# Kernel tuning notes

Hardware: AMD Instinct MI355X
Metric: run time of the kernel (lower is better)

Reference implementation:

```python
import jax, jax.numpy as jnp
import numpy as np

C_, A_, B_ = 1, 128, 128          # image_size
H, Z, T, N = 512, 128, 16, 32     # h_dim, z_dim, steps, attention grid
EPS = 1e-8
BATCH = 256
PATCH = C_ * N * N                # read/write patch size (C_=1)
IN_ENC = 2 * PATCH + H


def gru_cell(x, h, W_ih, W_hh, b_ih, b_hh):
    gi = x @ W_ih.T + b_ih
    gh = h @ W_hh.T + b_hh
    i_r, i_z, i_n = jnp.split(gi, 3, axis=-1)
    h_r, h_z, h_n = jnp.split(gh, 3, axis=-1)
    r = jax.nn.sigmoid(i_r + h_r)
    z = jax.nn.sigmoid(i_z + h_z)
    n = jnp.tanh(i_n + r * h_n)
    return (1.0 - z) * n + z * h


def filterbank(gt, delta, two_sigma_sq, num_pixels):
    # gt, delta: [b,1]; two_sigma_sq: [b,1,1]
    g = 0.5 * (num_pixels + 1) * (gt + 1.0)                       # [b,1]
    grid = jnp.arange(N, dtype=jnp.float32) - 0.5 * (N - 1)       # [N]
    mu = g + grid[None, :] * delta                                # [b,N]
    pix = jnp.arange(num_pixels, dtype=jnp.float32)               # [P]
    F = jnp.exp(-(pix[None, None, :] - mu[:, :, None]) ** 2 / two_sigma_sq)
    return F / jnp.maximum(F.sum(axis=-1, keepdims=True), EPS)    # [b,N,P]


def get_filterbanks(h_dec, W_attn, b_attn):
    p = h_dec @ W_attn.T + b_attn                                 # [b,5]
    gt_x, gt_y, log_ss, log_dt, log_g = [p[:, i:i + 1] for i in range(5)]
    two_sigma_sq = (2.0 * jnp.exp(log_ss))[:, :, None]            # [b,1,1]
    delta = (max(A_, B_) - 1) * jnp.exp(log_dt) / (N - 1)         # [b,1]
    gamma = jnp.exp(log_g)                                        # [b,1]
    F_x = filterbank(gt_x, delta, two_sigma_sq, A_)               # [b,N,A]
    F_y = filterbank(gt_y, delta, two_sigma_sq, B_)               # [b,N,B]
    return F_x, F_y, gamma


def draw_forward(x, eps, W_ih_enc, W_hh_enc, b_ih_enc, b_hh_enc,
                 W_ih_dec, W_hh_dec, b_ih_dec, b_hh_dec,
                 W_mu, b_mu, W_ls, b_ls, W_wr, b_wr,
                 W_ra, b_ra, W_wa, b_wa):
    b = x.shape[0]
    xf = x.reshape(b, -1)                                         # [b, A*B]
    reconsts0 = jnp.zeros_like(xf)
    h0 = jnp.zeros((b, H), dtype=xf.dtype)

    def step(carry, eps_t):
        reconsts, h_enc, h_dec = carry
        # NOTE: faithful to original: reconsts[-1] is last batch row, broadcast
        x_hat = xf - jax.nn.sigmoid(reconsts[-1])
        # ---- read with attention ----
        F_x, F_y, gamma = get_filterbanks(h_dec, W_ra, b_ra)
        F_x_t = jnp.swapaxes(F_x, -1, -2)                         # [b,A,N]
        img = xf.reshape(b, A_, B_)
        img_hat = x_hat.reshape(b, A_, B_)
        x_attn = (F_y @ img @ F_x_t).reshape(b, -1)               # [b,N*N]
        xh_attn = (F_y @ img_hat @ F_x_t).reshape(b, -1)
        r = gamma * jnp.concatenate([x_attn, xh_attn], axis=1)    # [b,2*N*N]
        # ---- encoder GRU ----
        h_enc = gru_cell(jnp.concatenate([r, h_dec], axis=1), h_enc,
                         W_ih_enc, W_hh_enc, b_ih_enc, b_hh_enc)
        # ---- sample z ~ Q ----
        mu = h_enc @ W_mu.T + b_mu
        sigma = jnp.exp(h_enc @ W_ls.T + b_ls)
        z = mu + eps_t * sigma
        # ---- decoder GRU ----
        h_dec = gru_cell(z, h_dec, W_ih_dec, W_hh_dec, b_ih_dec, b_hh_dec)
        # ---- write with attention ----
        F_xw, F_yw, gamma_w = get_filterbanks(h_dec, W_wa, b_wa)
        w = (h_dec @ W_wr.T + b_wr).reshape(b, N, N)
        wr = (jnp.swapaxes(F_yw, -1, -2) @ w @ F_xw).reshape(b, -1) / gamma_w
        return (reconsts + wr, h_enc, h_dec), None

    (reconsts, _, _), _ = jax.lax.scan(step, (reconsts0, h0, h0), eps)
    return jax.nn.sigmoid(reconsts).reshape(-1, C_, A_, B_)


def setup_inputs() -> dict:
    key = jax.random.key(0)
    ks = jax.random.split(key, 24)
    s = 0.02
    inp = {
        "x": jax.random.uniform(ks[0], (BATCH, C_, A_, B_), jnp.float32),
        "eps": jax.random.normal(ks[1], (T, BATCH, Z), jnp.float32),
        "W_ih_enc": jax.random.normal(ks[2], (3 * H, IN_ENC), jnp.float32) * s,
        "W_hh_enc": jax.random.normal(ks[3], (3 * H, H), jnp.float32) * s,
        "b_ih_enc": jnp.zeros((3 * H,), jnp.float32),
        "b_hh_enc": jnp.zeros((3 * H,), jnp.float32),
        "W_ih_dec": jax.random.normal(ks[4], (3 * H, Z), jnp.float32) * s,
        "W_hh_dec": jax.random.normal(ks[5], (3 * H, H), jnp.float32) * s,
        "b_ih_dec": jnp.zeros((3 * H,), jnp.float32),
        "b_hh_dec": jnp.zeros((3 * H,), jnp.float32),
        "W_mu": jax.random.normal(ks[6], (Z, H), jnp.float32) * s,
        "b_mu": jnp.zeros((Z,), jnp.float32),
        "W_ls": jax.random.normal(ks[7], (Z, H), jnp.float32) * s,
        "b_ls": jnp.zeros((Z,), jnp.float32),
        "W_wr": jax.random.normal(ks[8], (PATCH, H), jnp.float32) * s,
        "b_wr": jnp.zeros((PATCH,), jnp.float32),
        "W_ra": jax.random.normal(ks[9], (5, H), jnp.float32) * s,
        "b_ra": jnp.zeros((5,), jnp.float32),
        "W_wa": jax.random.normal(ks[10], (5, H), jnp.float32) * s,
        "b_wa": jnp.zeros((5,), jnp.float32),
    }
    return inp


def reference(x, eps, W_ih_enc, W_hh_enc, b_ih_enc, b_hh_enc,
              W_ih_dec, W_hh_dec, b_ih_dec, b_hh_dec,
              W_mu, b_mu, W_ls, b_ls, W_wr, b_wr,
              W_ra, b_ra, W_wa, b_wa):
    return draw_forward(x, eps, W_ih_enc, W_hh_enc, b_ih_enc, b_hh_enc,
                        W_ih_dec, W_hh_dec, b_ih_dec, b_hh_dec,
                        W_mu, b_mu, W_ls, b_ls, W_wr, b_wr,
                        W_ra, b_ra, W_wa, b_wa)
```

## Files before the change

### kernel.cpp

```cpp
#include <hip/hip_runtime.h>
#include <math.h>

#define BATCHN 256
#define HDIM 512
#define ZDIM 128
#define NGRID 32
#define ABDIM 128
#define IMGSZ 16384
#define ENCIN 2560
#define G3 1536
#define SPLITK 4

typedef __attribute__((ext_vector_type(8))) short short8;
typedef __attribute__((ext_vector_type(4))) float f32x4;

__device__ __forceinline__ float sigmoidf_(float x){ return 1.0f/(1.0f+expf(-x)); }

__device__ __forceinline__ ushort f2bf_rne(float f){
    union{float f; uint u;} x; x.f=f;
    uint r = (x.u + 0x7FFFu + ((x.u>>16)&1u)) >> 16;
    return (ushort)r;
}
__device__ __forceinline__ float bf2f(ushort h){
    union{uint u; float f;} y; y.u = ((uint)h)<<16;
    return y.f;
}

__global__ void init_slast_k(float* __restrict__ s_last){
    int i = blockIdx.x*256 + threadIdx.x;
    s_last[i] = 0.5f;
}

__global__ void conv_w_k(const float* __restrict__ W, ushort* __restrict__ Wh,
                         ushort* __restrict__ Wl, int n4){
    int i = blockIdx.x*256 + threadIdx.x;
    if(i>=n4) return;
    float4 v = ((const float4*)W)[i];
    float f[4] = {v.x, v.y, v.z, v.w};
    ushort h[4], l[4];
    #pragma unroll
    for(int j=0;j<4;j++){
        h[j] = f2bf_rne(f[j]);
        l[j] = f2bf_rne(f[j] - bf2f(h[j]));
    }
    ushort4 hv; hv.x=h[0]; hv.y=h[1]; hv.z=h[2]; hv.w=h[3];
    ushort4 lv; lv.x=l[0]; lv.y=l[1]; lv.z=l[2]; lv.w=l[3];
    ((ushort4*)Wh)[i] = hv;
    ((ushort4*)Wl)[i] = lv;
}

__device__ __forceinline__ void attn_params_dev512(const float* __restrict__ h,
        const float* __restrict__ W, const float* __restrict__ bvec,
        float* red5 , float* pp , int tid){
    float accp[5];
    #pragma unroll
    for(int i=0;i<5;i++) accp[i]=0.f;
    for(int k=tid;k<HDIM;k+=512){
        float hv = h[k];
        #pragma unroll
        for(int i=0;i<5;i++) accp[i] += hv*W[i*HDIM+k];
    }
    int wv = tid>>6;
    #pragma unroll
    for(int i=0;i<5;i++){
        float a = accp[i];
        #pragma unroll
        for(int o=32;o>0;o>>=1) a += __shfl_down(a,o);
        if((tid&63)==0) red5[i*8+wv]=a;
    }
    __syncthreads();
    if(tid<5){
        float s = bvec[tid];
        #pragma unroll
        for(int w2=0;w2<8;w2++) s += red5[tid*8+w2];
        pp[tid]=s;
    }
    __syncthreads();
}

__device__ __forceinline__ void fill_fb_T(float* fxT, float* fyT, const float* pp, int tid){
    float gx = 64.5f*(pp[0]+1.0f);
    float gy = 64.5f*(pp[1]+1.0f);
    float tss = 2.0f*expf(pp[2]);
    float delta = (127.0f/31.0f)*expf(pp[3]);
    int rr = tid>>3;
    int q  = tid&7;
    int j  = rr&31;
    bool isY = rr>=32;
    float mu = (isY?gy:gx) + ((float)j-15.5f)*delta;
    float v[16]; float s=0.f;
    #pragma unroll
    for(int i=0;i<16;i++){
        float d = (float)(q*16+i)-mu;
        float e = expf(-d*d/tss);
        v[i]=e; s+=e;
    }
    s += __shfl_xor(s,1); s += __shfl_xor(s,2); s += __shfl_xor(s,4);
    float inv = 1.0f/fmaxf(s,1e-8f);
    float* dst = isY? fyT : fxT;
    #pragma unroll
    for(int i=0;i<16;i++) dst[(q*16+i)*32 + j] = v[i]*inv;
    __syncthreads();
}

__device__ __forceinline__ void fill_fb_R(float (*fx)[ABDIM+1], float (*fy)[ABDIM+1], const float* pp, int tid){
    float gx = 64.5f*(pp[0]+1.0f);
    float gy = 64.5f*(pp[1]+1.0f);
    float tss = 2.0f*expf(pp[2]);
    float delta = (127.0f/31.0f)*expf(pp[3]);
    int rr = tid>>3;
    int q  = tid&7;
    int j  = rr&31;
    bool isY = rr>=32;
    float mu = (isY?gy:gx) + ((float)j-15.5f)*delta;
    float v[16]; float s=0.f;
    #pragma unroll
    for(int i=0;i<16;i++){
        float d = (float)(q*16+i)-mu;
        float e = expf(-d*d/tss);
        v[i]=e; s+=e;
    }
    s += __shfl_xor(s,1); s += __shfl_xor(s,2); s += __shfl_xor(s,4);
    float inv = 1.0f/fmaxf(s,1e-8f);
    float* rowp = isY? &fy[j][0] : &fx[j][0];
    #pragma unroll
    for(int i=0;i<16;i++) rowp[q*16+i] = v[i]*inv;
    __syncthreads();
}

__global__ __launch_bounds__(512) void read_attn_k(const float* __restrict__ xf, const float* __restrict__ s_last,
        const float* __restrict__ hdec, const ushort* __restrict__ Hd_h, const ushort* __restrict__ Hd_l,
        const float* __restrict__ W_ra, const float* __restrict__ b_ra,
        ushort* __restrict__ Eh, ushort* __restrict__ El){
    __shared__ float smem[4096 + 8256 + 48];
    float* sFxT = smem;
    float* sFyT = smem + 4096;
    float* tmp  = smem + 4096;
    float* red5 = smem + 4096 + 8256;
    float* pp   = red5 + 40;
    int bb = blockIdx.x; int tid = threadIdx.x;
    const float* h = hdec + bb*HDIM;
    attn_params_dev512(h, W_ra, b_ra, red5, pp, tid);
    float gamma = expf(pp[4]);
    fill_fb_T(sFxT, sFyT, pp, tid);

    const float* img = xf + (size_t)bb*IMGSZ;
    int c = tid & 127;
    int jg = tid >> 7;
    float acc0[8], accS[8];
    #pragma unroll
    for(int i=0;i<8;i++){ acc0[i]=0.f; accS[i]=0.f; }
    for(int k=0;k<ABDIM;k++){
        float s  = img[k*ABDIM + c];
        float sl = s_last[k*ABDIM + c];
        float4 f0 = *(const float4*)&sFyT[k*32 + jg*8];
        float4 f1 = *(const float4*)&sFyT[k*32 + jg*8 + 4];
        acc0[0]+=f0.x*s;  acc0[1]+=f0.y*s;  acc0[2]+=f0.z*s;  acc0[3]+=f0.w*s;
        acc0[4]+=f1.x*s;  acc0[5]+=f1.y*s;  acc0[6]+=f1.z*s;  acc0[7]+=f1.w*s;
        accS[0]+=f0.x*sl; accS[1]+=f0.y*sl; accS[2]+=f0.z*sl; accS[3]+=f0.w*sl;
        accS[4]+=f1.x*sl; accS[5]+=f1.y*sl; accS[6]+=f1.z*sl; accS[7]+=f1.w*sl;
    }
    __syncthreads();
    #pragma unroll
    for(int i=0;i<8;i++){
        int j = jg*8+i;
        tmp[0*32*129 + j*129 + c] = acc0[i];
        tmp[1*32*129 + j*129 + c] = acc0[i] - accS[i];
    }
    __syncthreads();
    {
        int i4 = tid & 7;
        int j  = (tid>>3) & 31;
        int p  = tid >> 8;
        float a0=0.f,a1=0.f,a2=0.f,a3=0.f;
        for(int cc=0; cc<ABDIM; cc++){
            float tv = tmp[p*32*129 + j*129 + cc];
            float4 fx = *(const float4*)&sFxT[cc*32 + i4*4];
            a0 += tv*fx.x; a1 += tv*fx.y; a2 += tv*fx.z; a3 += tv*fx.w;
        }
        float ov[4] = {gamma*a0, gamma*a1, gamma*a2, gamma*a3};
        ushort4 oh, ol;
        ushort hq;
        hq=f2bf_rne(ov[0]); oh.x=hq; ol.x=f2bf_rne(ov[0]-bf2f(hq));
        hq=f2bf_rne(ov[1]); oh.y=hq; ol.y=f2bf_rne(ov[1]-bf2f(hq));
        hq=f2bf_rne(ov[2]); oh.z=hq; ol.z=f2bf_rne(ov[2]-bf2f(hq));
        hq=f2bf_rne(ov[3]); oh.w=hq; ol.w=f2bf_rne(ov[3]-bf2f(hq));
        size_t off = (size_t)bb*ENCIN + p*1024 + j*NGRID + i4*4;
        *(ushort4*)(Eh + off) = oh;
        *(ushort4*)(El + off) = ol;
    }
    {
        int i = tid;
        Eh[(size_t)bb*ENCIN + 2048 + i] = Hd_h[(size_t)bb*HDIM + i];
        El[(size_t)bb*ENCIN + 2048 + i] = Hd_l[(size_t)bb*HDIM + i];
    }
}

__device__ __forceinline__ void gemm_one_bf(const ushort* __restrict__ Ah_g, const ushort* __restrict__ Al_g,
        const ushort* __restrict__ Wh, const ushort* __restrict__ Wl,
        int K, int s, int row0, int col0, int Nn, float* __restrict__ Out,
        ushort* Ah, ushort* Al, ushort* Bh, ushort* Bl, int tid){
    int lane = tid&63, w = tid>>6;
    int m0 = (w>>1)*32, n0 = (w&1)*32;
    int fr = lane&15, kq = (lane>>4)*8;
    int sr = tid>>2, sq = (tid&3)*16;
    int ch = K/SPLITK;
    int kend = (s+1)*ch;
    f32x4 acc[2][2];
    #pragma unroll
    for(int i=0;i<2;i++)
        #pragma unroll
        for(int j=0;j<2;j++) acc[i][j] = (f32x4){0.f,0.f,0.f,0.f};

    for(int k0=s*ch; k0<kend; k0+=64){
        int rem = kend - k0;
        uint4 vah0, vah1, val0, val1, vbh0, vbh1, vbl0, vbl1;
        bool gd = (sq < rem);
        if(gd){
            size_t aoff = (size_t)(row0+sr)*K + k0 + sq;
            size_t boff = (size_t)(col0+sr)*K + k0 + sq;
            vah0 = *(const uint4*)(Ah_g + aoff);
            vah1 = *(const uint4*)(Ah_g + aoff + 8);
            val0 = *(const uint4*)(Al_g + aoff);
            val1 = *(const uint4*)(Al_g + aoff + 8);
            vbh0 = *(const uint4*)(Wh + boff);
            vbh1 = *(const uint4*)(Wh + boff + 8);
            vbl0 = *(const uint4*)(Wl + boff);
            vbl1 = *(const uint4*)(Wl + boff + 8);
        }
        __syncthreads();
        if(gd){
            *(uint4*)&Ah[sr*72 + sq]     = vah0;
            *(uint4*)&Ah[sr*72 + sq + 8] = vah1;
            *(uint4*)&Al[sr*72 + sq]     = val0;
            *(uint4*)&Al[sr*72 + sq + 8] = val1;
            *(uint4*)&Bh[sr*72 + sq]     = vbh0;
            *(uint4*)&Bh[sr*72 + sq + 8] = vbh1;
            *(uint4*)&Bl[sr*72 + sq]     = vbl0;
            *(uint4*)&Bl[sr*72 + sq + 8] = vbl1;
        }
        __syncthreads();
        int nk = (rem>=64)?2:1;
        for(int ks=0; ks<nk; ks++){
            int kb = ks*32 + kq;
            short8 a_h[2], a_l[2], b_h[2], b_l[2];
            #pragma unroll
            for(int mf=0;mf<2;mf++){
                a_h[mf] = *(short8*)&Ah[(m0+mf*16+fr)*72 + kb];
                a_l[mf] = *(short8*)&Al[(m0+mf*16+fr)*72 + kb];
            }
            #pragma unroll
            for(int nf=0;nf<2;nf++){
                b_h[nf] = *(short8*)&Bh[(n0+nf*16+fr)*72 + kb];
                b_l[nf] = *(short8*)&Bl[(n0+nf*16+fr)*72 + kb];
            }
            #pragma unroll
            for(int mf=0;mf<2;mf++)
                #pragma unroll
                for(int nf=0;nf<2;nf++){
                    acc[mf][nf] = __builtin_amdgcn_mfma_f32_16x16x32_bf16(a_h[mf], b_h[nf], acc[mf][nf], 0,0,0);
                    acc[mf][nf] = __builtin_amdgcn_mfma_f32_16x16x32_bf16(a_h[mf], b_l[nf], acc[mf][nf], 0,0,0);
                    acc[mf][nf] = __builtin_amdgcn_mfma_f32_16x16x32_bf16(a_l[mf], b_h[nf], acc[mf][nf], 0,0,0);
                }
        }
    }
    int crow = (lane>>4)*4, ccol = lane&15;
    #pragma unroll
    for(int mf=0;mf<2;mf++)
        #pragma unroll
        for(int nf=0;nf<2;nf++)
            #pragma unroll
            for(int r=0;r<4;r++)
                Out[((size_t)s*BATCHN + row0+m0+mf*16+crow+r)*Nn + col0+n0+nf*16+ccol] = acc[mf][nf][r];
    __syncthreads();
}

__global__ __launch_bounds__(256) void gemm_bf_dual(
        const ushort* __restrict__ A1h, const ushort* __restrict__ A1l,
        const ushort* __restrict__ W1h, const ushort* __restrict__ W1l, int K1,
        const ushort* __restrict__ A2h, const ushort* __restrict__ A2l,
        const ushort* __restrict__ W2h, const ushort* __restrict__ W2l, int K2,
        float* __restrict__ Pi, float* __restrict__ Ph, int Nn){
    __shared__ ushort Ah[64*72], Al[64*72], Bh[64*72], Bl[64*72];
    int tid = threadIdx.x;
    int row0 = blockIdx.y*64, col0 = blockIdx.x*64, s = blockIdx.z;
    gemm_one_bf(A1h, A1l, W1h, W1l, K1, s, row0, col0, Nn, Pi, Ah, Al, Bh, Bl, tid);
    if(K2>0)
        gemm_one_bf(A2h, A2l, W2h, W2l, K2, s, row0, col0, Nn, Ph, Ah, Al, Bh, Bl, tid);
}

__global__ __launch_bounds__(512) void gru_combine_z_k(const float* __restrict__ Pi, const float* __restrict__ Ph,
        const float* __restrict__ bi, const float* __restrict__ bh,
        float* __restrict__ h, ushort* __restrict__ Hh, ushort* __restrict__ Hl,
        const float* __restrict__ Wmu, const float* __restrict__ bmu,
        const float* __restrict__ Wls, const float* __restrict__ bls,
        const float* __restrict__ eps_t, ushort* __restrict__ Zh, ushort* __restrict__ Zl){
    __shared__ float hs[HDIM];
    int bb = blockIdx.x, tid = threadIdx.x;
    int j = tid;
    float gi_r=bi[j], gi_z=bi[512+j], gi_n=bi[1024+j];
    float gh_r=bh[j], gh_z=bh[512+j], gh_n=bh[1024+j];
    #pragma unroll
    for(int s=0;s<SPLITK;s++){
        size_t base = ((size_t)s*BATCHN + bb)*G3 + j;
        gi_r += Pi[base]; gi_z += Pi[base+512]; gi_n += Pi[base+1024];
        gh_r += Ph[base]; gh_z += Ph[base+512]; gh_n += Ph[base+1024];
    }
    float r = sigmoidf_(gi_r + gh_r);
    float z = sigmoidf_(gi_z + gh_z);
    float n = tanhf(gi_n + r*gh_n);
    size_t hoff = (size_t)bb*HDIM + j;
    float hn = (1.f - z)*n + z*h[hoff];
    h[hoff] = hn; hs[j] = hn;
    ushort hh = f2bf_rne(hn);
    Hh[hoff] = hh; Hl[hoff] = f2bf_rne(hn - bf2f(hh));
    __syncthreads();
    int jo = tid>>2, l4 = tid&3;
    float am=0.f, al_=0.f;
    for(int k=l4;k<HDIM;k+=4){
        float hv = hs[k];
        am  += hv*Wmu[(size_t)jo*HDIM+k];
        al_ += hv*Wls[(size_t)jo*HDIM+k];
    }
    am  += __shfl_xor(am,1);  am  += __shfl_xor(am,2);
    al_ += __shfl_xor(al_,1); al_ += __shfl_xor(al_,2);
    if(l4==0){
        float mu = am + bmu[jo];
        float sg = expf(al_ + bls[jo]);
        float zv = mu + eps_t[(size_t)bb*ZDIM + jo]*sg;
        ushort zh = f2bf_rne(zv);
        Zh[(size_t)bb*ZDIM + jo] = zh;
        Zl[(size_t)bb*ZDIM + jo] = f2bf_rne(zv - bf2f(zh));
    }
}

__global__ void gru_combine_bf_k(const float* __restrict__ Pi, const float* __restrict__ Ph,
        const float* __restrict__ bi, const float* __restrict__ bh,
        float* __restrict__ h, ushort* __restrict__ Hh, ushort* __restrict__ Hl){
    int idx = blockIdx.x*256 + threadIdx.x;
    int bb = idx >> 9, j = idx & 511;
    float gi_r=bi[j], gi_z=bi[512+j], gi_n=bi[1024+j];
    float gh_r=bh[j], gh_z=bh[512+j], gh_n=bh[1024+j];
    #pragma unroll
    for(int s=0;s<SPLITK;s++){
        size_t base = ((size_t)s*BATCHN + bb)*G3 + j;
        gi_r += Pi[base]; gi_z += Pi[base+512]; gi_n += Pi[base+1024];
        gh_r += Ph[base]; gh_z += Ph[base+512]; gh_n += Ph[base+1024];
    }
    float r = sigmoidf_(gi_r + gh_r);
    float z = sigmoidf_(gi_z + gh_z);
    float n = tanhf(gi_n + r*gh_n);
    float hn = (1.f - z)*n + z*h[idx];
    h[idx] = hn;
    ushort hh = f2bf_rne(hn);
    Hh[idx] = hh; Hl[idx] = f2bf_rne(hn - bf2f(hh));
}

__global__ __launch_bounds__(512) void write_apply_k(const float* __restrict__ Pw, const float* __restrict__ b_wr,
        const float* __restrict__ hdec, const float* __restrict__ W_wa, const float* __restrict__ b_wa,
        float* __restrict__ rec, float* __restrict__ s_last){
    __shared__ float sFy[NGRID][ABDIM+1];
    __shared__ float sFx[NGRID][ABDIM+1];
    __shared__ float sw[NGRID][36];
    __shared__ float t[ABDIM][36];
    __shared__ float red5[40];
    __shared__ float pp[8];
    int bb = blockIdx.x, tid = threadIdx.x;
    const float* h = hdec + bb*HDIM;
    attn_params_dev512(h, W_wa, b_wa, red5, pp, tid);
    float invg = expf(-pp[4]);
    fill_fb_R(sFx, sFy, pp, tid);
    for(int i=tid;i<NGRID*NGRID;i+=512){
        float a = b_wr[i];
        #pragma unroll
        for(int s=0;s<SPLITK;s++) a += Pw[((size_t)s*BATCHN + bb)*1024 + i];
        sw[i>>5][i&31] = a;
    }
    __syncthreads();
    {
        int p = tid>>2, iq = tid&3;
        float a[8];
        #pragma unroll
        for(int i=0;i<8;i++) a[i]=0.f;
        for(int j=0;j<NGRID;j++){
            float fy = sFy[j][p];
            float4 w0 = *(const float4*)&sw[j][iq*8];
            float4 w1 = *(const float4*)&sw[j][iq*8+4];
            a[0]+=fy*w0.x; a[1]+=fy*w0.y; a[2]+=fy*w0.z; a[3]+=fy*w0.w;
            a[4]+=fy*w1.x; a[5]+=fy*w1.y; a[6]+=fy*w1.z; a[7]+=fy*w1.w;
        }
        float4 o0; o0.x=a[0];o0.y=a[1];o0.z=a[2];o0.w=a[3];
        float4 o1; o1.x=a[4];o1.y=a[5];o1.z=a[6];o1.w=a[7];
        *(float4*)&t[p][iq*8]   = o0;
        *(float4*)&t[p][iq*8+4] = o1;
    }
    __syncthreads();
    {
        int q = tid&127, pg = tid>>7;
        float fxc[32];
        #pragma unroll
        for(int i=0;i<32;i++) fxc[i] = sFx[i][q];
        for(int pi=0; pi<32; pi++){
            int p = pg*32 + pi;
            float acc = 0.f;
            #pragma unroll
            for(int i4=0;i4<8;i4++){
                float4 tv = *(const float4*)&t[p][i4*4];
                acc += tv.x*fxc[i4*4] + tv.y*fxc[i4*4+1] + tv.z*fxc[i4*4+2] + tv.w*fxc[i4*4+3];
            }
            size_t off = (size_t)bb*IMGSZ + p*ABDIM + q;
            float nv = rec[off] + acc*invg;
            rec[off] = nv;
            if(bb==BATCHN-1) s_last[p*ABDIM + q] = sigmoidf_(nv);
        }
    }
}

__global__ void sigmoid_all_k(float* __restrict__ rec){
    int i = blockIdx.x*256 + threadIdx.x;
    rec[i] = sigmoidf_(rec[i]);
}

extern "C" void kernel_launch(void* const* d_in, const int* in_sizes, int n_in,
                              void* d_out, int out_size, void* d_ws, size_t ws_size,
                              hipStream_t stream) {
    const float* x        = (const float*)d_in[0];
    const float* eps      = (const float*)d_in[1];
    const float* W_ih_enc = (const float*)d_in[2];
    const float* W_hh_enc = (const float*)d_in[3];
    const float* b_ih_enc = (const float*)d_in[4];
    const float* b_hh_enc = (const float*)d_in[5];
    const float* W_ih_dec = (const float*)d_in[6];
    const float* W_hh_dec = (const float*)d_in[7];
    const float* b_ih_dec = (const float*)d_in[8];
    const float* b_hh_dec = (const float*)d_in[9];
    const float* W_mu     = (const float*)d_in[10];
    const float* b_mu     = (const float*)d_in[11];
    const float* W_ls     = (const float*)d_in[12];
    const float* b_ls     = (const float*)d_in[13];
    const float* W_wr     = (const float*)d_in[14];
    const float* b_wr     = (const float*)d_in[15];
    const float* W_ra     = (const float*)d_in[16];
    const float* b_ra     = (const float*)d_in[17];
    const float* W_wa     = (const float*)d_in[18];
    const float* b_wa     = (const float*)d_in[19];

    float* rec = (float*)d_out;

    float* ws = (float*)d_ws;
    float* h_enc  = ws;  ws += BATCHN*HDIM;
    float* h_dec  = ws;  ws += BATCHN*HDIM;
    float* s_last = ws;  ws += IMGSZ;
    float* Pi     = ws;  ws += (size_t)SPLITK*BATCHN*G3;
    float* Ph     = ws;  ws += (size_t)SPLITK*BATCHN*G3;
    float* Pw     = Pi;

    ushort* us = (ushort*)ws;
    ushort* Wie_h = us; us += 1536*2560;
    ushort* Wie_l = us; us += 1536*2560;
    ushort* Whe_h = us; us += 1536*512;
    ushort* Whe_l = us; us += 1536*512;
    ushort* Wid_h = us; us += 1536*128;
    ushort* Wid_l = us; us += 1536*128;
    ushort* Whd_h = us; us += 1536*512;
    ushort* Whd_l = us; us += 1536*512;
    ushort* Wwr_h = us; us += 1024*512;
    ushort* Wwr_l = us; us += 1024*512;
    ushort* Eh    = us; us += BATCHN*ENCIN;
    ushort* El    = us; us += BATCHN*ENCIN;
    ushort* He_h  = us; us += BATCHN*HDIM;
    ushort* He_l  = us; us += BATCHN*HDIM;
    ushort* Hd_h  = us; us += BATCHN*HDIM;
    ushort* Hd_l  = us; us += BATCHN*HDIM;
    ushort* Zh    = us; us += BATCHN*ZDIM;
    ushort* Zl    = us; us += BATCHN*ZDIM;

    hipMemsetAsync(rec,   0, (size_t)BATCHN*IMGSZ*sizeof(float), stream);
    hipMemsetAsync(h_enc, 0, (size_t)BATCHN*HDIM*sizeof(float), stream);
    hipMemsetAsync(h_dec, 0, (size_t)BATCHN*HDIM*sizeof(float), stream);
    hipMemsetAsync(He_h,  0, (size_t)BATCHN*HDIM*sizeof(ushort)*2, stream);
    hipMemsetAsync(Hd_h,  0, (size_t)BATCHN*HDIM*sizeof(ushort)*2, stream);
    init_slast_k<<<IMGSZ/256,256,0,stream>>>(s_last);

    conv_w_k<<<(1536*2560/4+255)/256,256,0,stream>>>(W_ih_enc, Wie_h, Wie_l, 1536*2560/4);
    conv_w_k<<<(1536*512/4+255)/256,256,0,stream>>>(W_hh_enc, Whe_h, Whe_l, 1536*512/4);
    conv_w_k<<<(1536*128/4+255)/256,256,0,stream>>>(W_ih_dec, Wid_h, Wid_l, 1536*128/4);
    conv_w_k<<<(1536*512/4+255)/256,256,0,stream>>>(W_hh_dec, Whd_h, Whd_l, 1536*512/4);
    conv_w_k<<<(1024*512/4+255)/256,256,0,stream>>>(W_wr, Wwr_h, Wwr_l, 1024*512/4);

    for(int t=0;t<16;t++){
        read_attn_k<<<BATCHN,512,0,stream>>>(x, s_last, h_dec, Hd_h, Hd_l, W_ra, b_ra, Eh, El);
        gemm_bf_dual<<<dim3(G3/64, BATCHN/64, SPLITK),256,0,stream>>>(
            Eh, El, Wie_h, Wie_l, ENCIN, He_h, He_l, Whe_h, Whe_l, HDIM, Pi, Ph, G3);
        gru_combine_z_k<<<BATCHN,512,0,stream>>>(Pi, Ph, b_ih_enc, b_hh_enc,
            h_enc, He_h, He_l, W_mu, b_mu, W_ls, b_ls, eps + (size_t)t*BATCHN*ZDIM, Zh, Zl);
        gemm_bf_dual<<<dim3(G3/64, BATCHN/64, SPLITK),256,0,stream>>>(
            Zh, Zl, Wid_h, Wid_l, ZDIM, Hd_h, Hd_l, Whd_h, Whd_l, HDIM, Pi, Ph, G3);
        gru_combine_bf_k<<<BATCHN*HDIM/256,256,0,stream>>>(Pi, Ph, b_ih_dec, b_hh_dec, h_dec, Hd_h, Hd_l);
        gemm_bf_dual<<<dim3(1024/64, BATCHN/64, SPLITK),256,0,stream>>>(
            Hd_h, Hd_l, Wwr_h, Wwr_l, HDIM,
            (const ushort*)nullptr, (const ushort*)nullptr, (const ushort*)nullptr, (const ushort*)nullptr, 0,
            Pw, (float*)nullptr, 1024);
        write_apply_k<<<BATCHN,512,0,stream>>>(Pw, b_wr, h_dec, W_wa, b_wa, rec, s_last);
    }
    sigmoid_all_k<<<BATCHN*IMGSZ/256,256,0,stream>>>(rec);
}
```

Measured before the change: 1.694 ms.

## Merge encoder and decoder hidden GEMMs into one launch, fuse z-to-decoder input projection

The decoder's hidden-state GEMM (h_dec @ W_hh_dec) only depends on the previous h_dec, so it is now issued in the same launch as the encoder input and hidden GEMMs. A single job-indexed grid of 384 blocks replaces two dual-GEMM launches. The small z @ W_ih_dec.T projection (K=128) is computed in fp32 inside the encoder combine kernel, which removes a GEMM launch and the bf16 split of z and W_ih_dec. Split-K is reduced from 4 to 2 for the encoder input GEMM and dropped for the K=512 GEMMs, which cuts partial-sum traffic but gives each block a longer serial K loop. Fewer launches and less partial-sum reduction are traded against lower parallelism per GEMM and scalar fp32 work in the combine kernel.

```diff
diff --git a/kernel.cpp b/kernel.cpp
--- a/kernel.cpp
+++ b/kernel.cpp
@@ -9,7 +9,7 @@
 #define IMGSZ 16384
 #define ENCIN 2560
 #define G3 1536
-#define SPLITK 4
+#define SLAB (BATCHN*G3)
 
 typedef __attribute__((ext_vector_type(8))) short short8;
 typedef __attribute__((ext_vector_type(4))) float f32x4;
@@ -51,7 +51,7 @@
 
 __device__ __forceinline__ void attn_params_dev512(const float* __restrict__ h,
         const float* __restrict__ W, const float* __restrict__ bvec,
-        float* red5 , float* pp , int tid){
+        float* red5, float* pp, int tid){
     float accp[5];
     #pragma unroll
     for(int i=0;i<5;i++) accp[i]=0.f;
@@ -179,8 +179,7 @@
             a0 += tv*fx.x; a1 += tv*fx.y; a2 += tv*fx.z; a3 += tv*fx.w;
         }
         float ov[4] = {gamma*a0, gamma*a1, gamma*a2, gamma*a3};
-        ushort4 oh, ol;
-        ushort hq;
+        ushort4 oh, ol; ushort hq;
         hq=f2bf_rne(ov[0]); oh.x=hq; ol.x=f2bf_rne(ov[0]-bf2f(hq));
         hq=f2bf_rne(ov[1]); oh.y=hq; ol.y=f2bf_rne(ov[1]-bf2f(hq));
         hq=f2bf_rne(ov[2]); oh.z=hq; ol.z=f2bf_rne(ov[2]-bf2f(hq));
@@ -196,63 +195,54 @@
     }
 }
 
-__device__ __forceinline__ void gemm_one_bf(const ushort* __restrict__ Ah_g, const ushort* __restrict__ Al_g,
+__device__ void gemm_one(const ushort* __restrict__ Agh, const ushort* __restrict__ Agl,
         const ushort* __restrict__ Wh, const ushort* __restrict__ Wl,
-        int K, int s, int row0, int col0, int Nn, float* __restrict__ Out,
-        ushort* Ah, ushort* Al, ushort* Bh, ushort* Bl, int tid){
+        int K, int k0, int kiters, int row0, int col0, int Nn, float* __restrict__ Out,
+        ushort* AH, ushort* AL, ushort* BH, ushort* BL, int tid){
     int lane = tid&63, w = tid>>6;
     int m0 = (w>>1)*32, n0 = (w&1)*32;
     int fr = lane&15, kq = (lane>>4)*8;
     int sr = tid>>2, sq = (tid&3)*16;
-    int ch = K/SPLITK;
-    int kend = (s+1)*ch;
     f32x4 acc[2][2];
     #pragma unroll
     for(int i=0;i<2;i++)
         #pragma unroll
-        for(int j=0;j<2;j++) acc[i][j] = (f32x4){0.f,0.f,0.f,0.f};
-
-    for(int k0=s*ch; k0<kend; k0+=64){
-        int rem = kend - k0;
-        uint4 vah0, vah1, val0, val1, vbh0, vbh1, vbl0, vbl1;
-        bool gd = (sq < rem);
-        if(gd){
-            size_t aoff = (size_t)(row0+sr)*K + k0 + sq;
-            size_t boff = (size_t)(col0+sr)*K + k0 + sq;
-            vah0 = *(const uint4*)(Ah_g + aoff);
-            vah1 = *(const uint4*)(Ah_g + aoff + 8);
-            val0 = *(const uint4*)(Al_g + aoff);
-            val1 = *(const uint4*)(Al_g + aoff + 8);
-            vbh0 = *(const uint4*)(Wh + boff);
-            vbh1 = *(const uint4*)(Wh + boff + 8);
-            vbl0 = *(const uint4*)(Wl + boff);
-            vbl1 = *(const uint4*)(Wl + boff + 8);
-        }
+        for(int j=0;j<2;j++) acc[i][j]=(f32x4){0.f,0.f,0.f,0.f};
+    for(int it=0; it<kiters; ++it){
+        int kb = k0 + it*64;
+        size_t aoff = (size_t)(row0+sr)*K + kb + sq;
+        size_t boff = (size_t)(col0+sr)*K + kb + sq;
+        uint4 ah0 = *(const uint4*)(Agh + aoff);
+        uint4 ah1 = *(const uint4*)(Agh + aoff + 8);
+        uint4 al0 = *(const uint4*)(Agl + aoff);
+        uint4 al1 = *(const uint4*)(Agl + aoff + 8);
+        uint4 bh0 = *(const uint4*)(Wh + boff);
+        uint4 bh1 = *(const uint4*)(Wh + boff + 8);
+        uint4 bl0 = *(const uint4*)(Wl + boff);
+        uint4 bl1 = *(const uint4*)(Wl + boff + 8);
         __syncthreads();
-        if(gd){
-            *(uint4*)&Ah[sr*72 + sq]     = vah0;
-            *(uint4*)&Ah[sr*72 + sq + 8] = vah1;
-            *(uint4*)&Al[sr*72 + sq]     = val0;
-            *(uint4*)&Al[sr*72 + sq + 8] = val1;
-            *(uint4*)&Bh[sr*72 + sq]     = vbh0;
-            *(uint4*)&Bh[sr*72 + sq + 8] = vbh1;
-            *(uint4*)&Bl[sr*72 + sq]     = vbl0;
-            *(uint4*)&Bl[sr*72 + sq + 8] = vbl1;
-        }
+        *(uint4*)&AH[sr*72 + sq]     = ah0;
+        *(uint4*)&AH[sr*72 + sq + 8] = ah1;
+        *(uint4*)&AL[sr*72 + sq]     = al0;
+        *(uint4*)&AL[sr*72 + sq + 8] = al1;
+        *(uint4*)&BH[sr*72 + sq]     = bh0;
+        *(uint4*)&BH[sr*72 + sq + 8] = bh1;
+        *(uint4*)&BL[sr*72 + sq]     = bl0;
+        *(uint4*)&BL[sr*72 + sq + 8] = bl1;
         __syncthreads();
-        int nk = (rem>=64)?2:1;
-        for(int ks=0; ks<nk; ks++){
-            int kb = ks*32 + kq;
+        #pragma unroll
+        for(int ks=0; ks<2; ks++){
+            int kk = ks*32 + kq;
             short8 a_h[2], a_l[2], b_h[2], b_l[2];
             #pragma unroll
             for(int mf=0;mf<2;mf++){
-                a_h[mf] = *(short8*)&Ah[(m0+mf*16+fr)*72 + kb];
-                a_l[mf] = *(short8*)&Al[(m0+mf*16+fr)*72 + kb];
+                a_h[mf] = *(short8*)&AH[(m0+mf*16+fr)*72 + kk];
+                a_l[mf] = *(short8*)&AL[(m0+mf*16+fr)*72 + kk];
             }
             #pragma unroll
             for(int nf=0;nf<2;nf++){
-                b_h[nf] = *(short8*)&Bh[(n0+nf*16+fr)*72 + kb];
-                b_l[nf] = *(short8*)&Bl[(n0+nf*16+fr)*72 + kb];
+                b_h[nf] = *(short8*)&BH[(n0+nf*16+fr)*72 + kk];
+                b_l[nf] = *(short8*)&BL[(n0+nf*16+fr)*72 + kk];
             }
             #pragma unroll
             for(int mf=0;mf<2;mf++)
@@ -271,39 +261,73 @@
         for(int nf=0;nf<2;nf++)
             #pragma unroll
             for(int r=0;r<4;r++)
-                Out[((size_t)s*BATCHN + row0+m0+mf*16+crow+r)*Nn + col0+n0+nf*16+ccol] = acc[mf][nf][r];
-    __syncthreads();
-}
-
-__global__ __launch_bounds__(256) void gemm_bf_dual(
-        const ushort* __restrict__ A1h, const ushort* __restrict__ A1l,
-        const ushort* __restrict__ W1h, const ushort* __restrict__ W1l, int K1,
-        const ushort* __restrict__ A2h, const ushort* __restrict__ A2l,
-        const ushort* __restrict__ W2h, const ushort* __restrict__ W2l, int K2,
-        float* __restrict__ Pi, float* __restrict__ Ph, int Nn){
-    __shared__ ushort Ah[64*72], Al[64*72], Bh[64*72], Bl[64*72];
+                Out[(size_t)(row0+m0+mf*16+crow+r)*Nn + col0+n0+nf*16+ccol] = acc[mf][nf][r];
+}
+
+__global__ __launch_bounds__(256) void gemm3_k(
+        const ushort* __restrict__ Eh, const ushort* __restrict__ El,
+        const ushort* __restrict__ Wie_h, const ushort* __restrict__ Wie_l,
+        const ushort* __restrict__ He_h, const ushort* __restrict__ He_l,
+        const ushort* __restrict__ Whe_h, const ushort* __restrict__ Whe_l,
+        const ushort* __restrict__ Hd_h, const ushort* __restrict__ Hd_l,
+        const ushort* __restrict__ Whd_h, const ushort* __restrict__ Whd_l,
+        float* __restrict__ Pi, float* __restrict__ Ph, float* __restrict__ Ph2){
+    __shared__ ushort AH[64*72], AL[64*72], BH[64*72], BL[64*72];
+    int job = blockIdx.x, tid = threadIdx.x;
+    const ushort *Ah_,*Al_,*Wh_,*Wl_; int K_,k0_,ki_,r0_,c0_; float* Out_;
+    if(job < 192){
+        int tile = job % 96, s = job / 96;
+        Ah_=Eh; Al_=El; Wh_=Wie_h; Wl_=Wie_l;
+        K_=ENCIN; k0_=s*1280; ki_=20;
+        r0_=(tile/24)*64; c0_=(tile%24)*64;
+        Out_ = Pi + (size_t)s*SLAB;
+    } else if(job < 288){
+        int tile = job - 192;
+        Ah_=He_h; Al_=He_l; Wh_=Whe_h; Wl_=Whe_l;
+        K_=HDIM; k0_=0; ki_=8;
+        r0_=(tile/24)*64; c0_=(tile%24)*64;
+        Out_ = Ph;
+    } else {
+        int tile = job - 288;
+        Ah_=Hd_h; Al_=Hd_l; Wh_=Whd_h; Wl_=Whd_l;
+        K_=HDIM; k0_=0; ki_=8;
+        r0_=(tile/24)*64; c0_=(tile%24)*64;
+        Out_ = Ph2;
+    }
+    gemm_one(Ah_, Al_, Wh_, Wl_, K_, k0_, ki_, r0_, c0_, G3, Out_, AH, AL, BH, BL, tid);
+}
+
+__global__ __launch_bounds__(256) void gemm_wr_k(
+        const ushort* __restrict__ Hd_h, const ushort* __restrict__ Hd_l,
+        const ushort* __restrict__ Wwr_h, const ushort* __restrict__ Wwr_l,
+        float* __restrict__ Pw){
+    __shared__ ushort AH[64*72], AL[64*72], BH[64*72], BL[64*72];
     int tid = threadIdx.x;
-    int row0 = blockIdx.y*64, col0 = blockIdx.x*64, s = blockIdx.z;
-    gemm_one_bf(A1h, A1l, W1h, W1l, K1, s, row0, col0, Nn, Pi, Ah, Al, Bh, Bl, tid);
-    if(K2>0)
-        gemm_one_bf(A2h, A2l, W2h, W2l, K2, s, row0, col0, Nn, Ph, Ah, Al, Bh, Bl, tid);
-}
-
-__global__ __launch_bounds__(512) void gru_combine_z_k(const float* __restrict__ Pi, const float* __restrict__ Ph,
+    int r0 = blockIdx.y*64, c0 = blockIdx.x*64, s = blockIdx.z;
+    gemm_one(Hd_h, Hd_l, Wwr_h, Wwr_l, HDIM, s*128, 2, r0, c0, 1024,
+             Pw + (size_t)s*BATCHN*1024, AH, AL, BH, BL, tid);
+}
+
+__global__ __launch_bounds__(512) void combine_z_deci_k(const float* __restrict__ Pi, const float* __restrict__ Ph,
         const float* __restrict__ bi, const float* __restrict__ bh,
         float* __restrict__ h, ushort* __restrict__ Hh, ushort* __restrict__ Hl,
         const float* __restrict__ Wmu, const float* __restrict__ bmu,
         const float* __restrict__ Wls, const float* __restrict__ bls,
-        const float* __restrict__ eps_t, ushort* __restrict__ Zh, ushort* __restrict__ Zl){
+        const float* __restrict__ eps_t, const float* __restrict__ Wid,
+        float* __restrict__ gi_dec){
     __shared__ float hs[HDIM];
+    __shared__ float zs[ZDIM];
     int bb = blockIdx.x, tid = threadIdx.x;
     int j = tid;
     float gi_r=bi[j], gi_z=bi[512+j], gi_n=bi[1024+j];
     float gh_r=bh[j], gh_z=bh[512+j], gh_n=bh[1024+j];
     #pragma unroll
-    for(int s=0;s<SPLITK;s++){
-        size_t base = ((size_t)s*BATCHN + bb)*G3 + j;
+    for(int s=0;s<2;s++){
+        size_t base = (size_t)s*SLAB + (size_t)bb*G3 + j;
         gi_r += Pi[base]; gi_z += Pi[base+512]; gi_n += Pi[base+1024];
+    }
+    {
+        size_t base = (size_t)bb*G3 + j;
         gh_r += Ph[base]; gh_z += Ph[base+512]; gh_n += Ph[base+1024];
     }
     float r = sigmoidf_(gi_r + gh_r);
@@ -315,38 +339,49 @@
     ushort hh = f2bf_rne(hn);
     Hh[hoff] = hh; Hl[hoff] = f2bf_rne(hn - bf2f(hh));
     __syncthreads();
-    int jo = tid>>2, l4 = tid&3;
-    float am=0.f, al_=0.f;
-    for(int k=l4;k<HDIM;k+=4){
-        float hv = hs[k];
-        am  += hv*Wmu[(size_t)jo*HDIM+k];
-        al_ += hv*Wls[(size_t)jo*HDIM+k];
-    }
-    am  += __shfl_xor(am,1);  am  += __shfl_xor(am,2);
-    al_ += __shfl_xor(al_,1); al_ += __shfl_xor(al_,2);
-    if(l4==0){
-        float mu = am + bmu[jo];
-        float sg = expf(al_ + bls[jo]);
-        float zv = mu + eps_t[(size_t)bb*ZDIM + jo]*sg;
-        ushort zh = f2bf_rne(zv);
-        Zh[(size_t)bb*ZDIM + jo] = zh;
-        Zl[(size_t)bb*ZDIM + jo] = f2bf_rne(zv - bf2f(zh));
-    }
-}
-
-__global__ void gru_combine_bf_k(const float* __restrict__ Pi, const float* __restrict__ Ph,
+    {
+        int jo = tid>>2, l4 = tid&3;
+        float am=0.f, al_=0.f;
+        for(int k=l4;k<HDIM;k+=4){
+            float hv = hs[k];
+            am  += hv*Wmu[(size_t)jo*HDIM+k];
+            al_ += hv*Wls[(size_t)jo*HDIM+k];
+        }
+        am  += __shfl_xor(am,1);  am  += __shfl_xor(am,2);
+        al_ += __shfl_xor(al_,1); al_ += __shfl_xor(al_,2);
+        if(l4==0){
+            float mu = am + bmu[jo];
+            float sg = expf(al_ + bls[jo]);
+            zs[jo] = mu + eps_t[(size_t)bb*ZDIM + jo]*sg;
+        }
+    }
+    __syncthreads();
+    #pragma unroll
+    for(int rep=0; rep<3; rep++){
+        int nn = tid + rep*512;
+        const float4* wr = (const float4*)(Wid + (size_t)nn*ZDIM);
+        float a = 0.f;
+        #pragma unroll
+        for(int k4=0;k4<32;k4++){
+            float4 wv = wr[k4];
+            a += zs[k4*4]*wv.x + zs[k4*4+1]*wv.y + zs[k4*4+2]*wv.z + zs[k4*4+3]*wv.w;
+        }
+        gi_dec[(size_t)bb*G3 + nn] = a;
+    }
+}
+
+__global__ void combine_dec_k(const float* __restrict__ gi_dec, const float* __restrict__ Ph2,
         const float* __restrict__ bi, const float* __restrict__ bh,
         float* __restrict__ h, ushort* __restrict__ Hh, ushort* __restrict__ Hl){
     int idx = blockIdx.x*256 + threadIdx.x;
     int bb = idx >> 9, j = idx & 511;
-    float gi_r=bi[j], gi_z=bi[512+j], gi_n=bi[1024+j];
-    float gh_r=bh[j], gh_z=bh[512+j], gh_n=bh[1024+j];
-    #pragma unroll
-    for(int s=0;s<SPLITK;s++){
-        size_t base = ((size_t)s*BATCHN + bb)*G3 + j;
-        gi_r += Pi[base]; gi_z += Pi[base+512]; gi_n += Pi[base+1024];
-        gh_r += Ph[base]; gh_z += Ph[base+512]; gh_n += Ph[base+1024];
-    }
+    size_t base = (size_t)bb*G3 + j;
+    float gi_r = gi_dec[base]      + bi[j];
+    float gi_z = gi_dec[base+512]  + bi[512+j];
+    float gi_n = gi_dec[base+1024] + bi[1024+j];
+    float gh_r = Ph2[base]      + bh[j];
+    float gh_z = Ph2[base+512]  + bh[512+j];
+    float gh_n = Ph2[base+1024] + bh[1024+j];
     float r = sigmoidf_(gi_r + gh_r);
     float z = sigmoidf_(gi_z + gh_z);
     float n = tanhf(gi_n + r*gh_n);
@@ -373,7 +408,7 @@
     for(int i=tid;i<NGRID*NGRID;i+=512){
         float a = b_wr[i];
         #pragma unroll
-        for(int s=0;s<SPLITK;s++) a += Pw[((size_t)s*BATCHN + bb)*1024 + i];
+        for(int s=0;s<4;s++) a += Pw[((size_t)s*BATCHN + bb)*1024 + i];
         sw[i>>5][i&31] = a;
     }
     __syncthreads();
@@ -451,17 +486,17 @@
     float* h_enc  = ws;  ws += BATCHN*HDIM;
     float* h_dec  = ws;  ws += BATCHN*HDIM;
     float* s_last = ws;  ws += IMGSZ;
-    float* Pi     = ws;  ws += (size_t)SPLITK*BATCHN*G3;
-    float* Ph     = ws;  ws += (size_t)SPLITK*BATCHN*G3;
-    float* Pw     = Pi;
+    float* Pi     = ws;  ws += (size_t)2*SLAB;
+    float* Ph     = ws;  ws += (size_t)SLAB;
+    float* Ph2    = ws;  ws += (size_t)SLAB;
+    float* gi_dec = ws;  ws += (size_t)SLAB;
+    float* Pw     = ws;  ws += (size_t)4*BATCHN*1024;
 
     ushort* us = (ushort*)ws;
     ushort* Wie_h = us; us += 1536*2560;
     ushort* Wie_l = us; us += 1536*2560;
     ushort* Whe_h = us; us += 1536*512;
     ushort* Whe_l = us; us += 1536*512;
-    ushort* Wid_h = us; us += 1536*128;
-    ushort* Wid_l = us; us += 1536*128;
     ushort* Whd_h = us; us += 1536*512;
     ushort* Whd_l = us; us += 1536*512;
     ushort* Wwr_h = us; us += 1024*512;
@@ -472,8 +507,6 @@
     ushort* He_l  = us; us += BATCHN*HDIM;
     ushort* Hd_h  = us; us += BATCHN*HDIM;
     ushort* Hd_l  = us; us += BATCHN*HDIM;
-    ushort* Zh    = us; us += BATCHN*ZDIM;
-    ushort* Zl    = us; us += BATCHN*ZDIM;
 
     hipMemsetAsync(rec,   0, (size_t)BATCHN*IMGSZ*sizeof(float), stream);
     hipMemsetAsync(h_enc, 0, (size_t)BATCHN*HDIM*sizeof(float), stream);
@@ -484,23 +517,19 @@
 
     conv_w_k<<<(1536*2560/4+255)/256,256,0,stream>>>(W_ih_enc, Wie_h, Wie_l, 1536*2560/4);
     conv_w_k<<<(1536*512/4+255)/256,256,0,stream>>>(W_hh_enc, Whe_h, Whe_l, 1536*512/4);
-    conv_w_k<<<(1536*128/4+255)/256,256,0,stream>>>(W_ih_dec, Wid_h, Wid_l, 1536*128/4);
     conv_w_k<<<(1536*512/4+255)/256,256,0,stream>>>(W_hh_dec, Whd_h, Whd_l, 1536*512/4);
     conv_w_k<<<(1024*512/4+255)/256,256,0,stream>>>(W_wr, Wwr_h, Wwr_l, 1024*512/4);
 
     for(int t=0;t<16;t++){
         read_attn_k<<<BATCHN,512,0,stream>>>(x, s_last, h_dec, Hd_h, Hd_l, W_ra, b_ra, Eh, El);
-        gemm_bf_dual<<<dim3(G3/64, BATCHN/64, SPLITK),256,0,stream>>>(
-            Eh, El, Wie_h, Wie_l, ENCIN, He_h, He_l, Whe_h, Whe_l, HDIM, Pi, Ph, G3);
-        gru_combine_z_k<<<BATCHN,512,0,stream>>>(Pi, Ph, b_ih_enc, b_hh_enc,
-            h_enc, He_h, He_l, W_mu, b_mu, W_ls, b_ls, eps + (size_t)t*BATCHN*ZDIM, Zh, Zl);
-        gemm_bf_dual<<<dim3(G3/64, BATCHN/64, SPLITK),256,0,stream>>>(
-            Zh, Zl, Wid_h, Wid_l, ZDIM, Hd_h, Hd_l, Whd_h, Whd_l, HDIM, Pi, Ph, G3);
-        gru_combine_bf_k<<<BATCHN*HDIM/256,256,0,stream>>>(Pi, Ph, b_ih_dec, b_hh_dec, h_dec, Hd_h, Hd_l);
-        gemm_bf_dual<<<dim3(1024/64, BATCHN/64, SPLITK),256,0,stream>>>(
-            Hd_h, Hd_l, Wwr_h, Wwr_l, HDIM,
-            (const ushort*)nullptr, (const ushort*)nullptr, (const ushort*)nullptr, (const ushort*)nullptr, 0,
-            Pw, (float*)nullptr, 1024);
+        gemm3_k<<<384,256,0,stream>>>(Eh, El, Wie_h, Wie_l, He_h, He_l, Whe_h, Whe_l,
+                                      Hd_h, Hd_l, Whd_h, Whd_l, Pi, Ph, Ph2);
+        combine_z_deci_k<<<BATCHN,512,0,stream>>>(Pi, Ph, b_ih_enc, b_hh_enc,
+            h_enc, He_h, He_l, W_mu, b_mu, W_ls, b_ls, eps + (size_t)t*BATCHN*ZDIM,
+            W_ih_dec, gi_dec);
+        combine_dec_k<<<BATCHN*HDIM/256,256,0,stream>>>(gi_dec, Ph2, b_ih_dec, b_hh_dec,
+            h_dec, Hd_h, Hd_l);
+        gemm_wr_k<<<dim3(16,4,4),256,0,stream>>>(Hd_h, Hd_l, Wwr_h, Wwr_l, Pw);
         write_apply_k<<<BATCHN,512,0,stream>>>(Pw, b_wr, h_dec, W_wa, b_wa, rec, s_last);
     }
     sigmoid_all_k<<<BATCHN*IMGSZ/256,256,0,stream>>>(rec);
```

New measurement: 2.146 ms. 1.27x slower.
